# Optimization experiments

Measured on AMD Instinct MI355X. Metric: run time of the kernel, lower is better.

## Reference

```python
import jax, jax.numpy as jnp
import numpy as np

B, N, D, OUT, NUM_ITERS = 8, 4096, 1024, 1024, 3
LN_EPS = 1e-5


def setup_inputs() -> dict:
    key = jax.random.key(0)
    ks = jax.random.split(key, 8)
    s = (6.0 / (2 * D)) ** 0.5  # xavier-uniform-like scale
    return {
        "query": jax.random.normal(ks[0], (B, D), jnp.float32),
        "feat": jax.random.normal(ks[1], (B, N, D), jnp.float32),
        "W_h": jax.random.uniform(ks[2], (D, D), jnp.float32, -s, s),
        "W_f": jax.random.uniform(ks[3], (D, D), jnp.float32, -s, s),
        "W_g": jax.random.normal(ks[4], (4, D, D), jnp.float32) / np.sqrt(D),
        "ln_w": jnp.ones((D,), jnp.float32),
        "ln_b": jnp.zeros((D,), jnp.float32),
        "W_out": jax.random.uniform(ks[5], (OUT, D), jnp.float32, -s, s),
        "b_out": jnp.zeros((OUT,), jnp.float32),
        "feat_mask": jax.random.bernoulli(ks[6], 0.2, (B, 1, 1, N)),
    }


def _layer_norm(x, w, b):
    mu = x.mean(-1, keepdims=True)
    var = jnp.var(x, axis=-1, keepdims=True)
    return (x - mu) / jnp.sqrt(var + LN_EPS) * w + b


def reference(query, feat, W_h, W_f, W_g, ln_w, ln_b, W_out, b_out, feat_mask):
    q = query @ W_h                       # [B, D]
    f = feat @ W_f                        # [B, N, D]
    mask = feat_mask.reshape(feat.shape[0], feat.shape[1])  # squeeze(1).squeeze(1)
    b = jnp.where(mask, jnp.float32(-1e18), jnp.float32(0.0))  # [B, N]
    # feat_group is iteration-invariant: mean over the 4 orthogonal transforms
    # mean_g(f @ W_g[g].T) == f @ mean_g(W_g).T
    fg = f @ W_g.mean(0).T                # [B, N, D]
    n = fg.shape[1]
    for i in range(NUM_ITERS):
        c = jax.nn.softmax(b, axis=1)     # [B, N]
        if i == NUM_ITERS - 1:
            out = jnp.einsum('bn,bnd->bd', c, fg)
        else:
            delta = jnp.einsum('bd,bnd->bn', q, fg)
            delta = (delta - delta.mean(1, keepdims=True)) / (
                delta.std(1, keepdims=True, ddof=1) + 1e-9)  # torch.std is unbiased
            b = b + delta
            out = jnp.einsum('bn,bnd->bd', c, fg) / n  # mean over dim 1
        q = _layer_norm(q + jax.nn.selu(out), ln_w, ln_b)
    return q @ W_out.T + b_out
```

## Files before the change

### kernel.cpp

```cpp
#include <hip/hip_runtime.h>
#include <hip/hip_bf16.h>


using u16 = unsigned short;
using u32 = unsigned int;
using u8  = unsigned char;
using u64 = unsigned long long;

#define SELU_L 1.0507009873554805f
#define SELU_A 1.6732632423543772f

__device__ __align__(16) float g_M[1048576];
__device__ __align__(16) float g_q[8192];
__device__ __align__(16) float g_qc[8192];
__device__ __align__(16) float g_t[8192];
__device__ __align__(16) float g_u[8192];
__device__ __align__(16) float g_s[8192];
__device__ __align__(16) float g_bst[32768];
__device__ __align__(16) float g_c[32768];
__device__ __align__(16) float g_delta[32768];
__device__ __align__(16) float g_outv[8192];
__device__ __align__(16) float g_outv2[8192];
__device__ __align__(16) float g_v[8192];
__device__ int g_dt[12];

__device__ __forceinline__ float blo(u32 u){ return __uint_as_float(u << 16); }
__device__ __forceinline__ float bhi(u32 u){ return __uint_as_float(u & 0xffff0000u); }
__device__ __forceinline__ float b2f(u16 u){ return __uint_as_float(((u32)u) << 16); }

__device__ __forceinline__ void unpack8(uint4 x, float* f){
  f[0]=blo(x.x); f[1]=bhi(x.x); f[2]=blo(x.y); f[3]=bhi(x.y);
  f[4]=blo(x.z); f[5]=bhi(x.z); f[6]=blo(x.w); f[7]=bhi(x.w);
}

__device__ __forceinline__ float ldf(const void* p, size_t i, int dt){
  return dt ? ((const float*)p)[i] : b2f(((const u16*)p)[i]);
}
__device__ __forceinline__ void load8(const void* base, size_t idx, int dt, float* f){
  if (dt == 0) {
    uint4 x = *(const uint4*)((const u16*)base + idx);
    unpack8(x, f);
  } else {
    const float* p = (const float*)base + idx;
    float4 a = *(const float4*)p, b = *(const float4*)(p + 4);
    f[0]=a.x; f[1]=a.y; f[2]=a.z; f[3]=a.w; f[4]=b.x; f[5]=b.y; f[6]=b.z; f[7]=b.w;
  }
}

__device__ __forceinline__ float wredsum(float x){
#pragma unroll
  for (int o = 32; o; o >>= 1) x += __shfl_xor(x, o, 64);
  return x;
}

__device__ __forceinline__ bool mon(const u8* maskp, int e, int mode){
  if (mode == 0) return maskp[e] != 0;
  if (mode == 1) return ((const int*)maskp)[e] != 0;
  if (mode == 2 || mode == 4) return ((const u16*)maskp)[e] != 0;
  if (mode == 3) return ((const u32*)maskp)[e] != 0;
  return ((const u64*)maskp)[e] != 0ULL;
}

__global__ void kdet(const void* p0, const void* p1, const void* p2, const void* p3,
                     const void* p4, const void* p5, const void* p6, const void* p7,
                     const void* p8, const void* p9)
{
  const void* ps[10] = {p0,p1,p2,p3,p4,p5,p6,p7,p8,p9};
  int tid = threadIdx.x;
  int w = tid >> 6, lane = tid & 63;
  if (w < 9) {
    const u16* wp = (const u16*)ps[w];
    u16 x0 = wp[lane], x1 = wp[64 + lane];
    int e0 = (x0 >> 7) & 0xFF, e1 = (x1 >> 7) & 0xFF;
    u64 nz0 = __ballot(x0 != 0), nz1 = __ballot(x1 != 0);
    u64 pa0 = __ballot(x0 != 0 && e0 >= 0x70 && e0 <= 0x8F);
    u64 pa1 = __ballot(x1 != 0 && e1 >= 0x70 && e1 <= 0x8F);
    if (lane == 0) {
      const u64 evenm = 0x5555555555555555ULL;
      int nz = __popcll(nz0) + __popcll(nz1);
      int pass = __popcll(pa0) + __popcll(pa1);
      int evenNZ = __popcll(nz0 & evenm) + __popcll(nz1 & evenm);
      int oddNZ  = nz - evenNZ;
      int dt;
      if (nz == 0)                    dt = 0;
      else if (evenNZ == 0 && oddNZ)  dt = 1;
      else                            dt = (pass * 10 >= nz * 9) ? 0 : 1;
      g_dt[w] = dt;
    }
  } else if (w == 9) {
    const u8* mp = (const u8*)ps[9];
    u64 v = ((const u64*)mp)[lane];
    bool f16c=false, isF=false, nz01=false, nzNon4=false, nzM8_4=false, anynz=false;
#pragma unroll
    for (int j = 0; j < 8; ++j) {
      u8 cb = (u8)(v >> (8 * j));
      if (!cb) continue;
      int i = lane * 8 + j;
      anynz = true;
      if (cb == 0x3C && (i & 1)) f16c = true;
      if (cb == 0x3F || cb == 0x80) isF = true;
      int m = i & 3;
      if (m == 0 || m == 1) nz01 = true;
      if (m != 0) nzNon4 = true;
      if ((i & 7) == 4) nzM8_4 = true;
    }
    bool A  = __ballot(f16c)   != 0;
    bool Bf = __ballot(isF)    != 0;
    bool C  = __ballot(nz01)   != 0;
    bool Dn = __ballot(nzNon4) != 0;
    bool E  = __ballot(nzM8_4) != 0;
    bool F  = __ballot(anynz)  != 0;
    if (lane == 0) {
      int mode;
      if (A)       mode = 4;
      else if (Bf) mode = C ? 2 : 3;
      else if (Dn) mode = 0;
      else if (E)  mode = 1;
      else if (F)  mode = 5;
      else         mode = 1;
      g_dt[9] = mode;
    }
  }
  float4 z = make_float4(0.f, 0.f, 0.f, 0.f);
  for (int i = tid; i < 2048; i += 640) {
    ((float4*)g_q)[i] = z; ((float4*)g_t)[i] = z;
    ((float4*)g_u)[i] = z; ((float4*)g_s)[i] = z;
  }
}

__global__ void __launch_bounds__(256)
kprep(const void* __restrict__ Wg, const void* __restrict__ Wh,
      const void* __restrict__ query, const u8* __restrict__ maskp)
{
  __shared__ float wl[8192];
  __shared__ float ql[512];
  int blk = blockIdx.x, tid = threadIdx.x;
  if (blk < 512) {
    int dtg = g_dt[4];
    int e = blk * 2048 + tid * 8;
    float a[8] = {0,0,0,0,0,0,0,0};
#pragma unroll
    for (int g = 0; g < 4; ++g) {
      float f[8];
      load8(Wg, (size_t)g * 1048576 + e, dtg, f);
#pragma unroll
      for (int u = 0; u < 8; ++u) a[u] += f[u];
    }
    *(float4*)(g_M + e)     = make_float4(a[0]*0.25f, a[1]*0.25f, a[2]*0.25f, a[3]*0.25f);
    *(float4*)(g_M + e + 4) = make_float4(a[4]*0.25f, a[5]*0.25f, a[6]*0.25f, a[7]*0.25f);
  } else if (blk < 576) {
    int dtq = g_dt[0], dth = g_dt[2];
    int blk2 = blk - 512;
    int kt4 = blk2 & 3, dc = blk2 >> 2;
    for (int idx = tid; idx < 512; idx += 256) {
      int b = idx >> 6, dl = idx & 63;
      ql[idx] = ldf(query, b * 1024 + dc * 64 + dl, dtq);
    }
    float acc[8] = {0,0,0,0,0,0,0,0};
    int cq = tid & 31, r4 = tid >> 5;
#pragma unroll
    for (int h = 0; h < 2; ++h) {
      if (h) __syncthreads();
#pragma unroll
      for (int u4 = 0; u4 < 4; ++u4) {
        int r = r4 * 4 + u4;
        float f[8];
        load8(Wh, (size_t)(dc * 64 + h * 32 + r) * 1024 + kt4 * 256 + cq * 8, dth, f);
#pragma unroll
        for (int u = 0; u < 8; ++u) wl[r * 256 + cq * 8 + u] = f[u];
      }
      __syncthreads();
      for (int dd = 0; dd < 32; ++dd) {
        float w = wl[dd * 256 + tid];
        int dl = h * 32 + dd;
#pragma unroll
        for (int b = 0; b < 8; ++b) acc[b] += ql[(b << 6) + dl] * w;
      }
    }
    int k = kt4 * 256 + tid;
#pragma unroll
    for (int b = 0; b < 8; ++b) atomicAdd(&g_q[b * 1024 + k], acc[b]);
  } else if (blk < 608) {
    int mode = g_dt[9];
    int e0 = (blk - 576) * 1024 + tid * 4;
#pragma unroll
    for (int j = 0; j < 4; ++j) {
      int e = e0 + j;
      g_bst[e] = mon(maskp, e, mode) ? -1e18f : 0.f;
    }
  } else {
    __shared__ int sc[256];
    int mode = g_dt[9];
    int b = blk - 608;
    u32 bits = 0; int cnt = 0;
#pragma unroll
    for (int r = 0; r < 16; ++r) {
      int n = tid + 256 * r;
      bool on = mon(maskp, b * 4096 + n, mode);
      if (on) bits |= (1u << r); else ++cnt;
    }
    sc[tid] = cnt; __syncthreads();
    for (int s2 = 128; s2; s2 >>= 1) { if (tid < s2) sc[tid] += sc[tid + s2]; __syncthreads(); }
    int ct = sc[0];
    float inv = 1.f / (float)(ct ? ct : 4096);
    float moff = ct ? 0.f : inv;
#pragma unroll
    for (int r = 0; r < 16; ++r) {
      int n = tid + 256 * r;
      g_c[b * 4096 + n] = ((bits >> r) & 1u) ? moff : inv;
    }
  }
}

__device__ __forceinline__ void build_ql(float* ql, const float* qsrc,
                                         const float* osrc, float scale,
                                         const void* lnw, const void* lnb, int tid)
{
  int w = tid >> 6, lane = tid & 63;
  int dtw = g_dt[5], dtb = g_dt[6];
#pragma unroll
  for (int rr = 0; rr < 2; ++rr) {
    int b = w + rr * 4;
    const float* qb = qsrc + b * 1024;
    const float* ob = osrc + b * 1024;
    float x[16]; float sum = 0.f, sq = 0.f;
#pragma unroll
    for (int cc = 0; cc < 4; ++cc) {
      float4 qv = *(const float4*)(qb + cc * 256 + lane * 4);
      float4 ov = *(const float4*)(ob + cc * 256 + lane * 4);
      float q4[4] = {qv.x, qv.y, qv.z, qv.w};
      float o4[4] = {ov.x, ov.y, ov.z, ov.w};
#pragma unroll
      for (int e = 0; e < 4; ++e) {
        float o = o4[e] * scale;
        float se = (o > 0.f) ? SELU_L * o : SELU_L * SELU_A * expm1f(o);
        float val = q4[e] + se;
        x[cc * 4 + e] = val; sum += val; sq += val * val;
      }
    }
    sum = wredsum(sum); sq = wredsum(sq);
    float mean = sum * (1.f / 1024.f);
    float var = fmaxf(sq * (1.f / 1024.f) - mean * mean, 0.f);
    float rstd = rsqrtf(var + 1e-5f);
#pragma unroll
    for (int cc = 0; cc < 4; ++cc)
#pragma unroll
      for (int e = 0; e < 4; ++e) {
        int d = cc * 256 + lane * 4 + e;
        ql[b * 1024 + d] = (x[cc * 4 + e] - mean) * rstd * ldf(lnw, d, dtw)
                           + ldf(lnb, d, dtb);
      }
  }
  __syncthreads();
}

__global__ void __launch_bounds__(256)
kt(const void* __restrict__ lnw, const void* __restrict__ lnb, int phase)
{
  __shared__ __align__(16) float ql[8192];
  int blk = blockIdx.x, tid = threadIdx.x;
  if (blk >= 256) {
    int b = blk - 256;
    *(float4*)(g_u + b * 1024 + tid * 4) = make_float4(0.f, 0.f, 0.f, 0.f);
    return;
  }
  if (phase == 0) {
    for (int it = tid; it < 2048; it += 256)
      ((float4*)ql)[it] = ((const float4*)g_q)[it];
    __syncthreads();
  } else {
    build_ql(ql, g_qc, g_outv, 1.f / 4096.f, lnw, lnb, tid);
  }
  if (blk == 0) {
    for (int it = tid; it < 2048; it += 256)
      ((float4*)g_qc)[it] = ((const float4*)ql)[it];
  }
  int jt = blk & 3, dc4 = blk >> 2;
  int j = jt * 256 + tid;
  float acc[8] = {0,0,0,0,0,0,0,0};
  for (int dd = 0; dd < 16; ++dd) {
    int d = dc4 * 16 + dd;
    float mv = g_M[(size_t)d * 1024 + j];
#pragma unroll
    for (int b = 0; b < 8; ++b) acc[b] += ql[(b << 10) + d] * mv;
  }
#pragma unroll
  for (int b = 0; b < 8; ++b) atomicAdd(&g_t[b * 1024 + j], acc[b]);
}

__global__ void __launch_bounds__(256) kv(const void* __restrict__ Wf)
{
  __shared__ __align__(16) float shm[8192];
  int tid = threadIdx.x;
  int dtf = g_dt[3];
  for (int it = tid; it < 2048; it += 256)
    ((float4*)shm)[it] = ((const float4*)g_t)[it];
  __syncthreads();
  int w = tid >> 6, lane = tid & 63;
  int k = blockIdx.x * 4 + w;
  size_t row = (size_t)k * 1024;
  float f[16];
  load8(Wf, row + lane * 8, dtf, f);
  load8(Wf, row + 512 + lane * 8, dtf, f + 8);
  float acc[8];
#pragma unroll
  for (int b = 0; b < 8; ++b) {
    const float* tb = shm + b * 1024;
    float d = 0.f;
#pragma unroll
    for (int j = 0; j < 8; ++j) d += f[j]     * tb[lane * 8 + j];
#pragma unroll
    for (int j = 0; j < 8; ++j) d += f[8 + j] * tb[512 + lane * 8 + j];
    acc[b] = wredsum(d);
  }
  if (lane == 0) {
#pragma unroll
    for (int b = 0; b < 8; ++b) g_v[b * 1024 + k] = acc[b];
  }
}

__global__ void __launch_bounds__(256)
kfd(const void* __restrict__ feat, int need_delta)
{
  __shared__ float sl[4][1024];
  int blkx = blockIdx.x, tid = threadIdx.x;
  if (blkx >= 1024) {
    int b = blkx - 1024;
    *(float4*)(g_u + b * 1024 + tid * 4) = make_float4(0.f, 0.f, 0.f, 0.f);
    return;
  }
  int w = tid >> 6, lane = tid & 63;
  int b = blkx >> 7, ch = blkx & 127;
  int dtf = g_dt[1];
  float vr[16];
#pragma unroll
  for (int j = 0; j < 16; ++j) vr[j] = 0.f;
  if (need_delta) {
    const float* vb = g_v + b * 1024;
    float4 v0 = *(const float4*)(vb + lane * 8);
    float4 v1 = *(const float4*)(vb + lane * 8 + 4);
    float4 v2 = *(const float4*)(vb + 512 + lane * 8);
    float4 v3 = *(const float4*)(vb + 512 + lane * 8 + 4);
    vr[0]=v0.x; vr[1]=v0.y; vr[2]=v0.z; vr[3]=v0.w;
    vr[4]=v1.x; vr[5]=v1.y; vr[6]=v1.z; vr[7]=v1.w;
    vr[8]=v2.x; vr[9]=v2.y; vr[10]=v2.z; vr[11]=v2.w;
    vr[12]=v3.x; vr[13]=v3.y; vr[14]=v3.z; vr[15]=v3.w;
  }
  int n0 = ch * 32 + w * 8;
  float4 c0 = *(const float4*)(g_c + b * 4096 + n0);
  float4 c1 = *(const float4*)(g_c + b * 4096 + n0 + 4);
  float cc[8] = {c0.x, c0.y, c0.z, c0.w, c1.x, c1.y, c1.z, c1.w};
  float acc[16];
#pragma unroll
  for (int j = 0; j < 16; ++j) acc[j] = 0.f;
  for (int r = 0; r < 8; ++r) {
    int n = n0 + r;
    size_t row = ((size_t)b * 4096 + n) * 1024;
    float f[16];
    load8(feat, row + lane * 8, dtf, f);
    load8(feat, row + 512 + lane * 8, dtf, f + 8);
    float cn = cc[r];
#pragma unroll
    for (int j = 0; j < 16; ++j) acc[j] += cn * f[j];
    if (need_delta) {
      float dot = 0.f;
#pragma unroll
      for (int j = 0; j < 16; ++j) dot += f[j] * vr[j];
      dot = wredsum(dot);
      if (lane == 0) g_delta[b * 4096 + n] = dot;
    }
  }
#pragma unroll
  for (int j = 0; j < 8; ++j) {
    sl[w][lane * 8 + j] = acc[j];
    sl[w][512 + lane * 8 + j] = acc[8 + j];
  }
  __syncthreads();
#pragma unroll
  for (int j = 0; j < 4; ++j) {
    int k = tid * 4 + j;
    float val = sl[0][k] + sl[1][k] + sl[2][k] + sl[3][k];
    atomicAdd(&g_s[b * 1024 + k], val);
  }
}

__global__ void __launch_bounds__(256)
ksu(const void* __restrict__ Wf, int do_stats)
{
  __shared__ float sm[256];
  int blk = blockIdx.x, tid = threadIdx.x;
  if (blk < 8) {
    if (!do_stats) return;
    int b = blk;
    const float* drow = g_delta + b * 4096;
    float xs[16];
    float sum = 0.f, sq = 0.f;
#pragma unroll
    for (int rr = 0; rr < 4; ++rr) {
      float4 x4 = *(const float4*)(drow + tid * 4 + rr * 1024);
      float xx[4] = {x4.x, x4.y, x4.z, x4.w};
#pragma unroll
      for (int j = 0; j < 4; ++j) { xs[rr*4+j] = xx[j]; sum += xx[j]; sq += xx[j]*xx[j]; }
    }
    sm[tid] = sum; __syncthreads();
    for (int s2 = 128; s2; s2 >>= 1) { if (tid < s2) sm[tid] += sm[tid + s2]; __syncthreads(); }
    sum = sm[0]; __syncthreads();
    sm[tid] = sq; __syncthreads();
    for (int s2 = 128; s2; s2 >>= 1) { if (tid < s2) sm[tid] += sm[tid + s2]; __syncthreads(); }
    sq = sm[0]; __syncthreads();
    float mean = sum / 4096.f;
    float var = fmaxf((sq - 4096.f * mean * mean) / 4095.f, 0.f);
    float inv = 1.f / (sqrtf(var) + 1e-9f);
    float* brow = g_bst + b * 4096;
    float mx = -3.4e38f;
#pragma unroll
    for (int rr = 0; rr < 4; ++rr) {
      float4 b4 = *(const float4*)(brow + tid * 4 + rr * 1024);
      float bb[4] = {b4.x, b4.y, b4.z, b4.w};
#pragma unroll
      for (int j = 0; j < 4; ++j) {
        float nb = bb[j] + (xs[rr*4+j] - mean) * inv;
        xs[rr*4+j] = nb;
        mx = fmaxf(mx, nb);
      }
      *(float4*)(brow + tid * 4 + rr * 1024) =
          make_float4(xs[rr*4], xs[rr*4+1], xs[rr*4+2], xs[rr*4+3]);
    }
    sm[tid] = mx; __syncthreads();
    for (int s2 = 128; s2; s2 >>= 1) { if (tid < s2) sm[tid] = fmaxf(sm[tid], sm[tid + s2]); __syncthreads(); }
    mx = sm[0]; __syncthreads();
    float es = 0.f;
#pragma unroll
    for (int k16 = 0; k16 < 16; ++k16) { float e = __expf(xs[k16] - mx); xs[k16] = e; es += e; }
    sm[tid] = es; __syncthreads();
    for (int s2 = 128; s2; s2 >>= 1) { if (tid < s2) sm[tid] += sm[tid + s2]; __syncthreads(); }
    float cinv = 1.f / sm[0];
    float* crow = g_c + b * 4096;
#pragma unroll
    for (int rr = 0; rr < 4; ++rr)
      *(float4*)(crow + tid * 4 + rr * 1024) =
          make_float4(xs[rr*4]*cinv, xs[rr*4+1]*cinv, xs[rr*4+2]*cinv, xs[rr*4+3]*cinv);
    return;
  }
  int dtf = g_dt[3];
  int blk2 = blk - 8;
  int jt = blk2 & 3, kc4 = blk2 >> 2;
  if (tid < 128) {
    int b = tid >> 4, kk = tid & 15;
    sm[tid] = g_s[b * 1024 + kc4 * 16 + kk];
  }
  __syncthreads();
  int j = jt * 256 + tid;
  float acc[8] = {0,0,0,0,0,0,0,0};
  for (int kk = 0; kk < 16; ++kk) {
    int k = kc4 * 16 + kk;
    float w = ldf(Wf, (size_t)k * 1024 + j, dtf);
#pragma unroll
    for (int b = 0; b < 8; ++b) acc[b] += sm[(b << 4) + kk] * w;
  }
#pragma unroll
  for (int b = 0; b < 8; ++b) atomicAdd(&g_u[b * 1024 + j], acc[b]);
}

__global__ void __launch_bounds__(256) kout(int dst2)
{
  __shared__ __align__(16) float sh[8192];
  int blk = blockIdx.x, tid = threadIdx.x;
  if (blk >= 256) {
    if (blk < 264) {
      int b = blk - 256;
      *(float4*)(g_t + b * 1024 + tid * 4) = make_float4(0.f, 0.f, 0.f, 0.f);
    } else {
      int b = blk - 264;
      *(float4*)(g_s + b * 1024 + tid * 4) = make_float4(0.f, 0.f, 0.f, 0.f);
    }
    return;
  }
  float* dst = dst2 ? g_outv2 : g_outv;
  for (int it = tid; it < 2048; it += 256)
    ((float4*)sh)[it] = ((const float4*)g_u)[it];
  __syncthreads();
  int w = tid >> 6, lane = tid & 63;
  int d = blk * 4 + w;
  const float* row = g_M + (size_t)d * 1024;
  float f[16];
#pragma unroll
  for (int cc = 0; cc < 4; ++cc) {
    float4 x = *(const float4*)(row + cc * 256 + lane * 4);
    f[cc*4+0]=x.x; f[cc*4+1]=x.y; f[cc*4+2]=x.z; f[cc*4+3]=x.w;
  }
  float acc[8];
#pragma unroll
  for (int b = 0; b < 8; ++b) {
    const float* ub = sh + b * 1024;
    float dd = 0.f;
#pragma unroll
    for (int cc = 0; cc < 4; ++cc)
#pragma unroll
      for (int e = 0; e < 4; ++e) dd += f[cc * 4 + e] * ub[cc * 256 + lane * 4 + e];
    acc[b] = wredsum(dd);
  }
  if (lane == 0) {
#pragma unroll
    for (int b = 0; b < 8; ++b) dst[b * 1024 + d] = acc[b];
  }
}

__global__ void __launch_bounds__(256)
kfin(const void* __restrict__ Wout, const void* __restrict__ bout,
     const void* __restrict__ lnw, const void* __restrict__ lnb,
     float* __restrict__ out)
{
  __shared__ __align__(16) float ql[8192];
  int tid = threadIdx.x;
  build_ql(ql, g_qc, g_outv, 1.f / 4096.f, lnw, lnb, tid);
  build_ql(ql, ql, g_outv2, 1.f, lnw, lnb, tid);
  int w = tid >> 6, lane = tid & 63;
  int o = blockIdx.x * 4 + w;
  int dto = g_dt[7], dtb = g_dt[8];
  size_t row = (size_t)o * 1024;
  float f[16];
  load8(Wout, row + lane * 8, dto, f);
  load8(Wout, row + 512 + lane * 8, dto, f + 8);
  float acc[8];
#pragma unroll
  for (int b = 0; b < 8; ++b) {
    const float* qb = ql + b * 1024;
    float d = 0.f;
#pragma unroll
    for (int j = 0; j < 8; ++j) d += f[j]     * qb[lane * 8 + j];
#pragma unroll
    for (int j = 0; j < 8; ++j) d += f[8 + j] * qb[512 + lane * 8 + j];
    acc[b] = wredsum(d);
  }
  if (lane == 0) {
    float bo = ldf(bout, o, dtb);
#pragma unroll
    for (int b = 0; b < 8; ++b) out[b * 1024 + o] = acc[b] + bo;
  }
}

extern "C" void kernel_launch(void* const* d_in, const int* in_sizes, int n_in,
                              void* d_out, int out_size, void* d_ws, size_t ws_size,
                              hipStream_t stream)
{
  const void* query = d_in[0];
  const void* feat  = d_in[1];
  const void* Wh    = d_in[2];
  const void* Wf    = d_in[3];
  const void* Wg    = d_in[4];
  const void* lnw   = d_in[5];
  const void* lnb   = d_in[6];
  const void* Wout  = d_in[7];
  const void* bout  = d_in[8];
  const u8*   maskp = (const u8*)d_in[9];
  (void)in_sizes; (void)n_in; (void)out_size; (void)d_ws; (void)ws_size;

  kdet<<<1, 640, 0, stream>>>(query, feat, Wh, Wf, Wg, lnw, lnb, Wout, bout, maskp);
  kprep<<<616, 256, 0, stream>>>(Wg, Wh, query, maskp);

  kt<<<264, 256, 0, stream>>>(lnw, lnb, 0);
  kv<<<256, 256, 0, stream>>>(Wf);
  kfd<<<1024, 256, 0, stream>>>(feat, 1);
  ksu<<<264, 256, 0, stream>>>(Wf, 1);
  kout<<<272, 256, 0, stream>>>(0);
  kt<<<264, 256, 0, stream>>>(lnw, lnb, 1);
  kv<<<256, 256, 0, stream>>>(Wf);
  kfd<<<1024, 256, 0, stream>>>(feat, 1);
  ksu<<<264, 256, 0, stream>>>(Wf, 1);
  kout<<<272, 256, 0, stream>>>(0);
  kfd<<<1032, 256, 0, stream>>>(feat, 0);
  ksu<<<264, 256, 0, stream>>>(Wf, 0);
  kout<<<256, 256, 0, stream>>>(1);
  kfin<<<256, 256, 0, stream>>>(Wout, bout, lnw, lnb, (float*)d_out);
}
```

Before: 426.1 us.

## Precompute fused M·Wf product with split-bf16 MFMA, drop per-iteration Wf passes

Precomputes P = M·Wf^T once using a three-term split-bf16 MFMA GEMM, so each iteration applies one 1024x1024 matvec instead of separate M and Wf passes. kv/ksu kernels are removed and launches are fused into kvp/kpost with ping-pong s buffers. A sampled check kernel falls back to an FP32 recompute if accuracy is off. kfd now uses 512 blocks of 64 rows each. This adds an upfront GEMM of about 2 GFLOP plus conversion traffic in exchange for fewer dependent launches and fewer weight reads per iteration.

```diff
diff --git a/kernel.cpp b/kernel.cpp
--- a/kernel.cpp
+++ b/kernel.cpp
@@ -7,15 +7,23 @@
 using u8  = unsigned char;
 using u64 = unsigned long long;
 
+typedef short  bfrag __attribute__((ext_vector_type(8)));
+typedef float  f32x4 __attribute__((ext_vector_type(4)));
+typedef u16    u16x8 __attribute__((ext_vector_type(8)));
+
 #define SELU_L 1.0507009873554805f
 #define SELU_A 1.6732632423543772f
 
 __device__ __align__(16) float g_M[1048576];
+__device__ __align__(16) u16   g_Mh[1048576];
+__device__ __align__(16) u16   g_Ml[1048576];
+__device__ __align__(16) u16   g_Wh16[1048576];
+__device__ __align__(16) u16   g_Wl16[1048576];
+__device__ __align__(16) float g_P[1048576];
 __device__ __align__(16) float g_q[8192];
 __device__ __align__(16) float g_qc[8192];
-__device__ __align__(16) float g_t[8192];
-__device__ __align__(16) float g_u[8192];
-__device__ __align__(16) float g_s[8192];
+__device__ __align__(16) float g_s0[8192];
+__device__ __align__(16) float g_s1[8192];
 __device__ __align__(16) float g_bst[32768];
 __device__ __align__(16) float g_c[32768];
 __device__ __align__(16) float g_delta[32768];
@@ -23,6 +31,7 @@
 __device__ __align__(16) float g_outv2[8192];
 __device__ __align__(16) float g_v[8192];
 __device__ int g_dt[12];
+__device__ int g_flag[1];
 
 __device__ __forceinline__ float blo(u32 u){ return __uint_as_float(u << 16); }
 __device__ __forceinline__ float bhi(u32 u){ return __uint_as_float(u & 0xffff0000u); }
@@ -45,6 +54,13 @@
     float4 a = *(const float4*)p, b = *(const float4*)(p + 4);
     f[0]=a.x; f[1]=a.y; f[2]=a.z; f[3]=a.w; f[4]=b.x; f[5]=b.y; f[6]=b.z; f[7]=b.w;
   }
+}
+
+__device__ __forceinline__ void bsplit(float x, u16& h, u16& l){
+  u32 bits = __float_as_uint(x);
+  h = (u16)(bits >> 16);
+  float hf = __uint_as_float(bits & 0xffff0000u);
+  l = (u16)(__float_as_uint(x - hf) >> 16);
 }
 
 __device__ __forceinline__ float wredsum(float x){
@@ -123,14 +139,16 @@
   }
   float4 z = make_float4(0.f, 0.f, 0.f, 0.f);
   for (int i = tid; i < 2048; i += 640) {
-    ((float4*)g_q)[i] = z; ((float4*)g_t)[i] = z;
-    ((float4*)g_u)[i] = z; ((float4*)g_s)[i] = z;
-  }
+    ((float4*)g_q)[i] = z; ((float4*)g_v)[i] = z;
+    ((float4*)g_s0)[i] = z; ((float4*)g_s1)[i] = z;
+  }
+  if (tid == 0) g_flag[0] = 0;
 }
 
 __global__ void __launch_bounds__(256)
 kprep(const void* __restrict__ Wg, const void* __restrict__ Wh,
-      const void* __restrict__ query, const u8* __restrict__ maskp)
+      const void* __restrict__ query, const u8* __restrict__ maskp,
+      const void* __restrict__ Wf)
 {
   __shared__ float wl[8192];
   __shared__ float ql[512];
@@ -146,8 +164,17 @@
 #pragma unroll
       for (int u = 0; u < 8; ++u) a[u] += f[u];
     }
-    *(float4*)(g_M + e)     = make_float4(a[0]*0.25f, a[1]*0.25f, a[2]*0.25f, a[3]*0.25f);
-    *(float4*)(g_M + e + 4) = make_float4(a[4]*0.25f, a[5]*0.25f, a[6]*0.25f, a[7]*0.25f);
+    u16x8 hv, lv;
+#pragma unroll
+    for (int u = 0; u < 8; ++u) {
+      a[u] *= 0.25f;
+      u16 h, l; bsplit(a[u], h, l);
+      hv[u] = h; lv[u] = l;
+    }
+    *(float4*)(g_M + e)     = make_float4(a[0], a[1], a[2], a[3]);
+    *(float4*)(g_M + e + 4) = make_float4(a[4], a[5], a[6], a[7]);
+    *(u16x8*)(g_Mh + e) = hv;
+    *(u16x8*)(g_Ml + e) = lv;
   } else if (blk < 576) {
     int dtq = g_dt[0], dth = g_dt[2];
     int blk2 = blk - 512;
@@ -188,7 +215,7 @@
       int e = e0 + j;
       g_bst[e] = mon(maskp, e, mode) ? -1e18f : 0.f;
     }
-  } else {
+  } else if (blk < 616) {
     __shared__ int sc[256];
     int mode = g_dt[9];
     int b = blk - 608;
@@ -209,6 +236,95 @@
       int n = tid + 256 * r;
       g_c[b * 4096 + n] = ((bits >> r) & 1u) ? moff : inv;
     }
+  } else {
+    int dtf = g_dt[3];
+    int base = (blk - 616) * 4096 + tid * 16;
+    float f[16];
+    load8(Wf, base, dtf, f);
+    load8(Wf, base + 8, dtf, f + 8);
+    u16x8 hv0, lv0, hv1, lv1;
+#pragma unroll
+    for (int j = 0; j < 8; ++j) {
+      u16 h, l; bsplit(f[j], h, l); hv0[j] = h; lv0[j] = l;
+      bsplit(f[8 + j], h, l); hv1[j] = h; lv1[j] = l;
+    }
+    *(u16x8*)(g_Wh16 + base)     = hv0;
+    *(u16x8*)(g_Wl16 + base)     = lv0;
+    *(u16x8*)(g_Wh16 + base + 8) = hv1;
+    *(u16x8*)(g_Wl16 + base + 8) = lv1;
+  }
+}
+
+__global__ void __launch_bounds__(256) kPm()
+{
+  int tid = threadIdx.x, w = tid >> 6, lane = tid & 63;
+  int tile = blockIdx.x * 4 + w;
+  int dp0 = (tile >> 6) * 16;
+  int d0  = (tile & 63) * 16;
+  int rc = lane & 15, kg = lane >> 4;
+  const u16* mh = g_Mh   + (size_t)(dp0 + rc) * 1024 + kg * 8;
+  const u16* ml = g_Ml   + (size_t)(dp0 + rc) * 1024 + kg * 8;
+  const u16* wh = g_Wh16 + (size_t)(d0 + rc) * 1024 + kg * 8;
+  const u16* wlp= g_Wl16 + (size_t)(d0 + rc) * 1024 + kg * 8;
+  f32x4 acc = {0.f, 0.f, 0.f, 0.f};
+  for (int k0 = 0; k0 < 1024; k0 += 32) {
+    bfrag ah = *(const bfrag*)(mh + k0);
+    bfrag al = *(const bfrag*)(ml + k0);
+    bfrag bh = *(const bfrag*)(wh + k0);
+    bfrag bl = *(const bfrag*)(wlp + k0);
+    acc = __builtin_amdgcn_mfma_f32_16x16x32_bf16(ah, bh, acc, 0, 0, 0);
+    acc = __builtin_amdgcn_mfma_f32_16x16x32_bf16(al, bh, acc, 0, 0, 0);
+    acc = __builtin_amdgcn_mfma_f32_16x16x32_bf16(ah, bl, acc, 0, 0, 0);
+  }
+#pragma unroll
+  for (int j = 0; j < 4; ++j)
+    g_P[(size_t)(dp0 + kg * 4 + j) * 1024 + d0 + rc] = acc[j];
+}
+
+__global__ void kPchk(const void* __restrict__ Wf)
+{
+  int tid = threadIdx.x;
+  int dtf = g_dt[3];
+  int dp = (tid * 97) & 1023;
+  int d  = (tid * 61 + 511) & 1023;
+  const float* mrow = g_M + (size_t)dp * 1024;
+  float ref = 0.f;
+  for (int k = 0; k < 1024; k += 8) {
+    float f[8];
+    load8(Wf, (size_t)d * 1024 + k, dtf, f);
+#pragma unroll
+    for (int j = 0; j < 8; ++j) ref += f[j] * mrow[k + j];
+  }
+  float got = g_P[(size_t)dp * 1024 + d];
+  bool bad = fabsf(got - ref) > 0.02f * (fabsf(ref) + 0.01f);
+  if (__ballot(bad) != 0ULL && (tid & 63) == 0) g_flag[0] = 1;
+}
+
+__global__ void __launch_bounds__(256) kPfix(const void* __restrict__ Wf)
+{
+  if (g_flag[0] == 0) return;
+  __shared__ float mrow[4096];
+  int blk = blockIdx.x, tid = threadIdx.x;
+  int dtf = g_dt[3];
+  for (int i = tid; i < 4096; i += 256)
+    mrow[i] = g_M[(size_t)(blk * 4 + (i >> 10)) * 1024 + (i & 1023)];
+  __syncthreads();
+  for (int dd = tid; dd < 1024; dd += 256) {
+    float a0 = 0.f, a1 = 0.f, a2 = 0.f, a3 = 0.f;
+    for (int k = 0; k < 1024; k += 8) {
+      float f[8];
+      load8(Wf, (size_t)dd * 1024 + k, dtf, f);
+#pragma unroll
+      for (int j = 0; j < 8; ++j) {
+        float x = f[j];
+        a0 += x * mrow[k + j];        a1 += x * mrow[1024 + k + j];
+        a2 += x * mrow[2048 + k + j]; a3 += x * mrow[3072 + k + j];
+      }
+    }
+    g_P[(size_t)(blk * 4 + 0) * 1024 + dd] = a0;
+    g_P[(size_t)(blk * 4 + 1) * 1024 + dd] = a1;
+    g_P[(size_t)(blk * 4 + 2) * 1024 + dd] = a2;
+    g_P[(size_t)(blk * 4 + 3) * 1024 + dd] = a3;
   }
 }
 
@@ -255,13 +371,13 @@
 }
 
 __global__ void __launch_bounds__(256)
-kt(const void* __restrict__ lnw, const void* __restrict__ lnb, int phase)
+kvp(const void* __restrict__ lnw, const void* __restrict__ lnb, int phase)
 {
   __shared__ __align__(16) float ql[8192];
   int blk = blockIdx.x, tid = threadIdx.x;
   if (blk >= 256) {
     int b = blk - 256;
-    *(float4*)(g_u + b * 1024 + tid * 4) = make_float4(0.f, 0.f, 0.f, 0.f);
+    *(float4*)(g_s0 + b * 1024 + tid * 4) = make_float4(0.f, 0.f, 0.f, 0.f);
     return;
   }
   if (phase == 0) {
@@ -279,87 +395,43 @@
   int j = jt * 256 + tid;
   float acc[8] = {0,0,0,0,0,0,0,0};
   for (int dd = 0; dd < 16; ++dd) {
-    int d = dc4 * 16 + dd;
-    float mv = g_M[(size_t)d * 1024 + j];
-#pragma unroll
-    for (int b = 0; b < 8; ++b) acc[b] += ql[(b << 10) + d] * mv;
-  }
-#pragma unroll
-  for (int b = 0; b < 8; ++b) atomicAdd(&g_t[b * 1024 + j], acc[b]);
-}
-
-__global__ void __launch_bounds__(256) kv(const void* __restrict__ Wf)
-{
-  __shared__ __align__(16) float shm[8192];
-  int tid = threadIdx.x;
-  int dtf = g_dt[3];
-  for (int it = tid; it < 2048; it += 256)
-    ((float4*)shm)[it] = ((const float4*)g_t)[it];
-  __syncthreads();
-  int w = tid >> 6, lane = tid & 63;
-  int k = blockIdx.x * 4 + w;
-  size_t row = (size_t)k * 1024;
-  float f[16];
-  load8(Wf, row + lane * 8, dtf, f);
-  load8(Wf, row + 512 + lane * 8, dtf, f + 8);
-  float acc[8];
-#pragma unroll
-  for (int b = 0; b < 8; ++b) {
-    const float* tb = shm + b * 1024;
-    float d = 0.f;
-#pragma unroll
-    for (int j = 0; j < 8; ++j) d += f[j]     * tb[lane * 8 + j];
-#pragma unroll
-    for (int j = 0; j < 8; ++j) d += f[8 + j] * tb[512 + lane * 8 + j];
-    acc[b] = wredsum(d);
-  }
-  if (lane == 0) {
-#pragma unroll
-    for (int b = 0; b < 8; ++b) g_v[b * 1024 + k] = acc[b];
-  }
+    int dp = dc4 * 16 + dd;
+    float pv = g_P[(size_t)dp * 1024 + j];
+#pragma unroll
+    for (int b = 0; b < 8; ++b) acc[b] += ql[(b << 10) + dp] * pv;
+  }
+#pragma unroll
+  for (int b = 0; b < 8; ++b) atomicAdd(&g_v[b * 1024 + j], acc[b]);
 }
 
 __global__ void __launch_bounds__(256)
-kfd(const void* __restrict__ feat, int need_delta)
+kfd(const void* __restrict__ feat, int need_delta, int sflag)
 {
   __shared__ float sl[4][1024];
   int blkx = blockIdx.x, tid = threadIdx.x;
-  if (blkx >= 1024) {
-    int b = blkx - 1024;
-    *(float4*)(g_u + b * 1024 + tid * 4) = make_float4(0.f, 0.f, 0.f, 0.f);
-    return;
-  }
+  float* s = sflag ? g_s1 : g_s0;
   int w = tid >> 6, lane = tid & 63;
-  int b = blkx >> 7, ch = blkx & 127;
+  int b = blkx >> 6, ch = blkx & 63;
   int dtf = g_dt[1];
   float vr[16];
 #pragma unroll
   for (int j = 0; j < 16; ++j) vr[j] = 0.f;
   if (need_delta) {
     const float* vb = g_v + b * 1024;
-    float4 v0 = *(const float4*)(vb + lane * 8);
-    float4 v1 = *(const float4*)(vb + lane * 8 + 4);
-    float4 v2 = *(const float4*)(vb + 512 + lane * 8);
-    float4 v3 = *(const float4*)(vb + 512 + lane * 8 + 4);
-    vr[0]=v0.x; vr[1]=v0.y; vr[2]=v0.z; vr[3]=v0.w;
-    vr[4]=v1.x; vr[5]=v1.y; vr[6]=v1.z; vr[7]=v1.w;
-    vr[8]=v2.x; vr[9]=v2.y; vr[10]=v2.z; vr[11]=v2.w;
-    vr[12]=v3.x; vr[13]=v3.y; vr[14]=v3.z; vr[15]=v3.w;
-  }
-  int n0 = ch * 32 + w * 8;
-  float4 c0 = *(const float4*)(g_c + b * 4096 + n0);
-  float4 c1 = *(const float4*)(g_c + b * 4096 + n0 + 4);
-  float cc[8] = {c0.x, c0.y, c0.z, c0.w, c1.x, c1.y, c1.z, c1.w};
+#pragma unroll
+    for (int j = 0; j < 8; ++j) { vr[j] = vb[lane * 8 + j]; vr[8 + j] = vb[512 + lane * 8 + j]; }
+  }
   float acc[16];
 #pragma unroll
   for (int j = 0; j < 16; ++j) acc[j] = 0.f;
-  for (int r = 0; r < 8; ++r) {
+  int n0 = ch * 64 + w * 16;
+  for (int r = 0; r < 16; ++r) {
     int n = n0 + r;
     size_t row = ((size_t)b * 4096 + n) * 1024;
     float f[16];
     load8(feat, row + lane * 8, dtf, f);
     load8(feat, row + 512 + lane * 8, dtf, f + 8);
-    float cn = cc[r];
+    float cn = g_c[b * 4096 + n];
 #pragma unroll
     for (int j = 0; j < 16; ++j) acc[j] += cn * f[j];
     if (need_delta) {
@@ -380,14 +452,14 @@
   for (int j = 0; j < 4; ++j) {
     int k = tid * 4 + j;
     float val = sl[0][k] + sl[1][k] + sl[2][k] + sl[3][k];
-    atomicAdd(&g_s[b * 1024 + k], val);
+    atomicAdd(&s[b * 1024 + k], val);
   }
 }
 
 __global__ void __launch_bounds__(256)
-ksu(const void* __restrict__ Wf, int do_stats)
-{
-  __shared__ float sm[256];
+kpost(int do_stats, int sflag, int dst2)
+{
+  __shared__ __align__(16) float sh[8192];
   int blk = blockIdx.x, tid = threadIdx.x;
   if (blk < 8) {
     if (!do_stats) return;
@@ -402,12 +474,12 @@
 #pragma unroll
       for (int j = 0; j < 4; ++j) { xs[rr*4+j] = xx[j]; sum += xx[j]; sq += xx[j]*xx[j]; }
     }
-    sm[tid] = sum; __syncthreads();
-    for (int s2 = 128; s2; s2 >>= 1) { if (tid < s2) sm[tid] += sm[tid + s2]; __syncthreads(); }
-    sum = sm[0]; __syncthreads();
-    sm[tid] = sq; __syncthreads();
-    for (int s2 = 128; s2; s2 >>= 1) { if (tid < s2) sm[tid] += sm[tid + s2]; __syncthreads(); }
-    sq = sm[0]; __syncthreads();
+    sh[tid] = sum; __syncthreads();
+    for (int s2 = 128; s2; s2 >>= 1) { if (tid < s2) sh[tid] += sh[tid + s2]; __syncthreads(); }
+    sum = sh[0]; __syncthreads();
+    sh[tid] = sq; __syncthreads();
+    for (int s2 = 128; s2; s2 >>= 1) { if (tid < s2) sh[tid] += sh[tid + s2]; __syncthreads(); }
+    sq = sh[0]; __syncthreads();
     float mean = sum / 4096.f;
     float var = fmaxf((sq - 4096.f * mean * mean) / 4095.f, 0.f);
     float inv = 1.f / (sqrtf(var) + 1e-9f);
@@ -426,15 +498,15 @@
       *(float4*)(brow + tid * 4 + rr * 1024) =
           make_float4(xs[rr*4], xs[rr*4+1], xs[rr*4+2], xs[rr*4+3]);
     }
-    sm[tid] = mx; __syncthreads();
-    for (int s2 = 128; s2; s2 >>= 1) { if (tid < s2) sm[tid] = fmaxf(sm[tid], sm[tid + s2]); __syncthreads(); }
-    mx = sm[0]; __syncthreads();
+    sh[tid] = mx; __syncthreads();
+    for (int s2 = 128; s2; s2 >>= 1) { if (tid < s2) sh[tid] = fmaxf(sh[tid], sh[tid + s2]); __syncthreads(); }
+    mx = sh[0]; __syncthreads();
     float es = 0.f;
 #pragma unroll
     for (int k16 = 0; k16 < 16; ++k16) { float e = __expf(xs[k16] - mx); xs[k16] = e; es += e; }
-    sm[tid] = es; __syncthreads();
-    for (int s2 = 128; s2; s2 >>= 1) { if (tid < s2) sm[tid] += sm[tid + s2]; __syncthreads(); }
-    float cinv = 1.f / sm[0];
+    sh[tid] = es; __syncthreads();
+    for (int s2 = 128; s2; s2 >>= 1) { if (tid < s2) sh[tid] += sh[tid + s2]; __syncthreads(); }
+    float cinv = 1.f / sh[0];
     float* crow = g_c + b * 4096;
 #pragma unroll
     for (int rr = 0; rr < 4; ++rr)
@@ -442,47 +514,19 @@
           make_float4(xs[rr*4]*cinv, xs[rr*4+1]*cinv, xs[rr*4+2]*cinv, xs[rr*4+3]*cinv);
     return;
   }
-  int dtf = g_dt[3];
-  int blk2 = blk - 8;
-  int jt = blk2 & 3, kc4 = blk2 >> 2;
-  if (tid < 128) {
-    int b = tid >> 4, kk = tid & 15;
-    sm[tid] = g_s[b * 1024 + kc4 * 16 + kk];
-  }
-  __syncthreads();
-  int j = jt * 256 + tid;
-  float acc[8] = {0,0,0,0,0,0,0,0};
-  for (int kk = 0; kk < 16; ++kk) {
-    int k = kc4 * 16 + kk;
-    float w = ldf(Wf, (size_t)k * 1024 + j, dtf);
-#pragma unroll
-    for (int b = 0; b < 8; ++b) acc[b] += sm[(b << 4) + kk] * w;
-  }
-#pragma unroll
-  for (int b = 0; b < 8; ++b) atomicAdd(&g_u[b * 1024 + j], acc[b]);
-}
-
-__global__ void __launch_bounds__(256) kout(int dst2)
-{
-  __shared__ __align__(16) float sh[8192];
-  int blk = blockIdx.x, tid = threadIdx.x;
-  if (blk >= 256) {
-    if (blk < 264) {
-      int b = blk - 256;
-      *(float4*)(g_t + b * 1024 + tid * 4) = make_float4(0.f, 0.f, 0.f, 0.f);
-    } else {
-      int b = blk - 264;
-      *(float4*)(g_s + b * 1024 + tid * 4) = make_float4(0.f, 0.f, 0.f, 0.f);
-    }
+  if (blk >= 264) {
+    int b = blk - 264;
+    *(float4*)(g_v + b * 1024 + tid * 4) = make_float4(0.f, 0.f, 0.f, 0.f);
     return;
   }
+  const float* s = sflag ? g_s1 : g_s0;
   float* dst = dst2 ? g_outv2 : g_outv;
   for (int it = tid; it < 2048; it += 256)
-    ((float4*)sh)[it] = ((const float4*)g_u)[it];
+    ((float4*)sh)[it] = ((const float4*)s)[it];
   __syncthreads();
   int w = tid >> 6, lane = tid & 63;
-  int d = blk * 4 + w;
-  const float* row = g_M + (size_t)d * 1024;
+  int dp = (blk - 8) * 4 + w;
+  const float* row = g_P + (size_t)dp * 1024;
   float f[16];
 #pragma unroll
   for (int cc = 0; cc < 4; ++cc) {
@@ -502,7 +546,7 @@
   }
   if (lane == 0) {
 #pragma unroll
-    for (int b = 0; b < 8; ++b) dst[b * 1024 + d] = acc[b];
+    for (int b = 0; b < 8; ++b) dst[b * 1024 + dp] = acc[b];
   }
 }
 
@@ -557,20 +601,18 @@
   (void)in_sizes; (void)n_in; (void)out_size; (void)d_ws; (void)ws_size;
 
   kdet<<<1, 640, 0, stream>>>(query, feat, Wh, Wf, Wg, lnw, lnb, Wout, bout, maskp);
-  kprep<<<616, 256, 0, stream>>>(Wg, Wh, query, maskp);
-
-  kt<<<264, 256, 0, stream>>>(lnw, lnb, 0);
-  kv<<<256, 256, 0, stream>>>(Wf);
-  kfd<<<1024, 256, 0, stream>>>(feat, 1);
-  ksu<<<264, 256, 0, stream>>>(Wf, 1);
-  kout<<<272, 256, 0, stream>>>(0);
-  kt<<<264, 256, 0, stream>>>(lnw, lnb, 1);
-  kv<<<256, 256, 0, stream>>>(Wf);
-  kfd<<<1024, 256, 0, stream>>>(feat, 1);
-  ksu<<<264, 256, 0, stream>>>(Wf, 1);
-  kout<<<272, 256, 0, stream>>>(0);
-  kfd<<<1032, 256, 0, stream>>>(feat, 0);
-  ksu<<<264, 256, 0, stream>>>(Wf, 0);
-  kout<<<256, 256, 0, stream>>>(1);
+  kprep<<<872, 256, 0, stream>>>(Wg, Wh, query, maskp, Wf);
+  kPm<<<1024, 256, 0, stream>>>();
+  kPchk<<<1, 256, 0, stream>>>(Wf);
+  kPfix<<<256, 256, 0, stream>>>(Wf);
+
+  kvp<<<256, 256, 0, stream>>>(lnw, lnb, 0);
+  kfd<<<512, 256, 0, stream>>>(feat, 1, 0);
+  kpost<<<272, 256, 0, stream>>>(1, 0, 0);
+  kvp<<<264, 256, 0, stream>>>(lnw, lnb, 1);
+  kfd<<<512, 256, 0, stream>>>(feat, 1, 1);
+  kpost<<<264, 256, 0, stream>>>(1, 1, 0);
+  kfd<<<512, 256, 0, stream>>>(feat, 0, 0);
+  kpost<<<264, 256, 0, stream>>>(0, 0, 1);
   kfin<<<256, 256, 0, stream>>>(Wout, bout, lnw, lnb, (float*)d_out);
 }
```

Result: slower. 517.8 us (+21.5%).
